# Optimization experiments

Measured on AMD Instinct MI355X. Metric: run time of the kernel, lower is better.

Reference implementation:

```python
import jax, jax.numpy as jnp
import numpy as np

# Dims: B=4, C_in=256, H=W=64 -> L=4096, token_dim D=256, state_dim N=512, K=4
B_, C_IN, H_, W_ = 4, 256, 64, 64
D, N, K = 256, 512, 4


def setup_inputs() -> dict:
    key = jax.random.key(0)
    ks = jax.random.split(key, 16)
    g = lambda k, shape, sc=0.02: (jax.random.normal(k, shape, jnp.float32) * sc)
    return {
        'feat_map': jax.random.normal(ks[0], (B_, C_IN, H_, W_), jnp.float32),
        'hf_map':   jax.random.normal(ks[1], (B_, C_IN, H_, W_), jnp.float32),
        # 1x1 conv proj_f / proj_hf: weight (out=D, in=C_IN), bias (D,)
        'Wf':  g(ks[2], (D, C_IN)), 'bf':  jnp.zeros((D,), jnp.float32),
        'Whf': g(ks[3], (D, C_IN)), 'bhf': jnp.zeros((D,), jnp.float32),
        # alpha_head: Linear(D, D//2) -> GELU -> Linear(D//2, K)
        'Wa1': g(ks[4], (D // 2, D)), 'ba1': jnp.zeros((D // 2,), jnp.float32),
        'Wa2': g(ks[5], (K, D // 2)), 'ba2': jnp.zeros((K,), jnp.float32),
        # SelectiveSSM base tuples: diagonal decay logits A (K,N), input maps B (K,N,D), output maps C (K,D,N)
        'A_base': g(ks[6], (K, N), 1.0),
        'B_base': g(ks[7], (K, N, D), 0.02),
        'C_base': g(ks[8], (K, D, N), 0.02),
        # out_proj 1x1 conv: (C_IN, D)
        'Wout': g(ks[9], (C_IN, D)), 'bout': jnp.zeros((C_IN,), jnp.float32),
    }


def _stage(feat_map, hf_map, Wf, bf, Whf, bhf, Wa1, ba1, Wa2, ba2,
           A_base, B_base, C_base, Wout, bout):
    B, C, H, W = feat_map.shape
    L = H * W
    # 1x1 conv token projections -> (B, L, D)
    t_f = jnp.einsum('bchw,dc->bdhw', feat_map, Wf) + bf[None, :, None, None]
    t_hf = jnp.einsum('bchw,dc->bdhw', hf_map, Whf) + bhf[None, :, None, None]
    x = t_f.reshape(B, -1, L).transpose(0, 2, 1)        # (B, L, D)
    t_hf_seq = t_hf.reshape(B, -1, L).transpose(0, 2, 1)  # (B, L, D)
    # gating MLP -> per-token mixture weights over K base SSMs
    hmid = jax.nn.gelu(t_hf_seq @ Wa1.T + ba1, approximate=False)
    alpha = jax.nn.softmax(hmid @ Wa2.T + ba2, axis=-1)  # (B, L, K)
    # selective SSM: per-token mixed diagonal decay and input drive
    a = jax.nn.sigmoid(jnp.einsum('blk,kn->bln', alpha, A_base))   # (B, L, N)
    u = jnp.einsum('bld,blk,knd->bln', x, alpha, B_base)           # (B, L, N)

    def step(h, au):
        a_t, u_t = au                   # each (B, N)
        h = a_t * h + u_t
        return h, h

    h0 = jnp.zeros((B, a.shape[-1]), x.dtype)
    _, hs = jax.lax.scan(step, h0, (a.transpose(1, 0, 2), u.transpose(1, 0, 2)))
    h_seq = hs.transpose(1, 0, 2)                                   # (B, L, N)
    # mixed readout
    y = jnp.einsum('blk,bln,kdn->bld', alpha, h_seq, C_base)        # (B, L, D)
    y_map = y.transpose(0, 2, 1).reshape(B, -1, H, W)
    out = jnp.einsum('bdhw,cd->bchw', y_map, Wout) + bout[None, :, None, None]
    return out


def reference(feat_map, hf_map, Wf, bf, Whf, bhf, Wa1, ba1, Wa2, ba2,
              A_base, B_base, C_base, Wout, bout):
    return _stage(feat_map, hf_map, Wf, bf, Whf, bhf, Wa1, ba1, Wa2, ba2,
                  A_base, B_base, C_base, Wout, bout)
```

## Files before the change

### kernel.cpp

```cpp
#include <hip/hip_runtime.h>
#include <hip/hip_bf16.h>
#include <math.h>

#define B_  4
#define CIN 256
#define L_  4096
#define D_  256
#define N_  512
#define K_  4
#define DH  128
#define BL  (B_ * L_)

#define NCHUNK 128
#define CLEN   (L_ / NCHUNK)

typedef __attribute__((ext_vector_type(8))) short bfrag;
typedef __attribute__((ext_vector_type(4))) float f4;

__device__ __forceinline__ float bf2f(unsigned short u) {
  return __uint_as_float(((unsigned int)u) << 16);
}
__device__ __forceinline__ unsigned short f2bf(float f) {
  unsigned int u = __float_as_uint(f);
  return (unsigned short)((u + 0x7FFFu + ((u >> 16) & 1u)) >> 16);
}

__global__ void k_prep(const float* __restrict__ Wf, const float* __restrict__ Whf,
                       const float* __restrict__ Wa1, const float* __restrict__ Wout,
                       const float* __restrict__ Bb, const float* __restrict__ Cb,
                       const float* __restrict__ bfv, const float* __restrict__ bhfv,
                       unsigned short* __restrict__ Wfb ,
                       unsigned short* __restrict__ Wa1b,
                       unsigned short* __restrict__ Woutb,
                       unsigned short* __restrict__ Bb16,
                       unsigned short* __restrict__ Cb16,
                       float* __restrict__ biascat) {
  int i = blockIdx.x * 256 + threadIdx.x;
  if (i < 65536) { Wfb[i] = f2bf(Wf[i]); return; } i -= 65536;
  if (i < 65536) { Wfb[65536 + i] = f2bf(Whf[i]); return; } i -= 65536;
  if (i < 32768) { Wa1b[i] = f2bf(Wa1[i]); return; } i -= 32768;
  if (i < 65536) { Woutb[i] = f2bf(Wout[i]); return; } i -= 65536;
  if (i < 524288) {
    int d = i & 255, n = (i >> 8) & 511, k = i >> 17;
    Bb16[(((size_t)n << 2) | k) << 8 | d] = f2bf(Bb[i]);
    return;
  } i -= 524288;
  if (i < 524288) {
    int nn = i & 511, d = (i >> 9) & 255, k = i >> 17;
    Cb16[(((size_t)d << 2) | k) << 9 | nn] = f2bf(Cb[i]);
    return;
  } i -= 524288;
  if (i < 256) { biascat[i] = bfv[i]; return; } i -= 256;
  if (i < 256) { biascat[256 + i] = bhfv[i]; }
}

__global__ void k_transpose2(const float* __restrict__ feat, const float* __restrict__ hf,
                             unsigned short* __restrict__ featT ) {
  __shared__ float tile[32][33];
  const int z = blockIdx.z;
  const int b = z & 3, which = z >> 2;
  const float* in = which ? hf : feat;
  unsigned short* outT = featT + (size_t)which * BL * CIN;
  const int l0 = blockIdx.x * 32, c0 = blockIdx.y * 32;
  const int tx = threadIdx.x, ty = threadIdx.y;
  const float* p = in + ((size_t)b * CIN + c0 + ty) * L_ + l0 + tx;
#pragma unroll
  for (int i = 0; i < 32; i += 8) tile[ty + i][tx] = p[(size_t)i * L_];
  __syncthreads();
  unsigned short* q = outT + ((size_t)b * L_ + l0 + ty) * CIN + c0 + tx;
#pragma unroll
  for (int i = 0; i < 32; i += 8) q[(size_t)i * CIN] = f2bf(tile[tx][ty + i]);
}

__global__ void k_alpha(const float* __restrict__ hm0, const float* __restrict__ hm1,
                        const float* __restrict__ ba1, const float* __restrict__ Wa2,
                        const float* __restrict__ ba2, float* __restrict__ alpha) {
  __shared__ float w2[K_ * DH];
  __shared__ float b1[DH];
  __shared__ float b2[K_];
  for (int i = threadIdx.x; i < K_ * DH; i += 256) w2[i] = Wa2[i];
  if (threadIdx.x < DH) b1[threadIdx.x] = ba1[threadIdx.x];
  if (threadIdx.x < K_) b2[threadIdx.x] = ba2[threadIdx.x];
  __syncthreads();
  const int token = blockIdx.x * 64 + (threadIdx.x >> 2);
  const int q = threadIdx.x & 3;
  float a0 = 0.f, a1 = 0.f, a2 = 0.f, a3 = 0.f;
  const size_t base = (size_t)token * DH + q * 32;
#pragma unroll
  for (int j4 = 0; j4 < 8; ++j4) {
    float4 h0 = *(const float4*)(hm0 + base + j4 * 4);
    float4 h1 = *(const float4*)(hm1 + base + j4 * 4);
    const float hv[4] = {h0.x + h1.x, h0.y + h1.y, h0.z + h1.z, h0.w + h1.w};
#pragma unroll
    for (int e = 0; e < 4; ++e) {
      const int d = q * 32 + j4 * 4 + e;
      float g = hv[e] + b1[d];
      g = 0.5f * g * (1.0f + erff(g * 0.70710678118654752f));
      a0 += g * w2[0 * DH + d];
      a1 += g * w2[1 * DH + d];
      a2 += g * w2[2 * DH + d];
      a3 += g * w2[3 * DH + d];
    }
  }
  a0 += __shfl_xor(a0, 1); a1 += __shfl_xor(a1, 1); a2 += __shfl_xor(a2, 1); a3 += __shfl_xor(a3, 1);
  a0 += __shfl_xor(a0, 2); a1 += __shfl_xor(a1, 2); a2 += __shfl_xor(a2, 2); a3 += __shfl_xor(a3, 2);
  a0 += b2[0]; a1 += b2[1]; a2 += b2[2]; a3 += b2[3];
  float m = fmaxf(fmaxf(a0, a1), fmaxf(a2, a3));
  float e0 = expf(a0 - m), e1 = expf(a1 - m), e2 = expf(a2 - m), e3 = expf(a3 - m);
  float inv = 1.f / (e0 + e1 + e2 + e3);
  float my = (q == 0) ? e0 : (q == 1) ? e1 : (q == 2) ? e2 : e3;
  alpha[(size_t)token * 4 + q] = my * inv;
}


__global__ void k_scanA(const float* __restrict__ u, const float* __restrict__ alpha,
                        const float* __restrict__ Abase,
                        float* __restrict__ P, float* __restrict__ Hend) {
  const int n = threadIdx.x;
  const int bc = blockIdx.x;
  const int b = bc >> 7, c = bc & 127;
  const float A0 = Abase[n], A1 = Abase[N_ + n], A2 = Abase[2 * N_ + n], A3 = Abase[3 * N_ + n];
  const size_t tok0 = (size_t)b * L_ + (size_t)c * CLEN;
  float p = 1.f, h = 0.f;
  for (int l = 0; l < CLEN; ++l) {
    const size_t t = tok0 + l;
    float4 al = *(const float4*)(alpha + t * 4);
    float s = al.x * A0 + al.y * A1 + al.z * A2 + al.w * A3;
    float av = 1.f / (1.f + expf(-s));
    float uv = u[t * N_ + n];
    h = av * h + uv;
    p *= av;
  }
  P[(size_t)bc * N_ + n] = p;
  Hend[(size_t)bc * N_ + n] = h;
}

__global__ void k_scanB(const float* __restrict__ P, const float* __restrict__ Hend,
                        float* __restrict__ Hstart) {
  const int n = threadIdx.x;
  const int b = blockIdx.x;
  float h = 0.f;
  for (int c = 0; c < NCHUNK; ++c) {
    size_t idx = ((size_t)b * NCHUNK + c) * N_ + n;
    Hstart[idx] = h;
    h = P[idx] * h + Hend[idx];
  }
}

__global__ void k_scanC(const float* __restrict__ u, const float* __restrict__ alpha,
                        const float* __restrict__ Abase, const float* __restrict__ Hstart,
                        unsigned short* __restrict__ hbf) {
  const int n = threadIdx.x;
  const int bc = blockIdx.x;
  const int b = bc >> 7, c = bc & 127;
  const float A0 = Abase[n], A1 = Abase[N_ + n], A2 = Abase[2 * N_ + n], A3 = Abase[3 * N_ + n];
  const size_t tok0 = (size_t)b * L_ + (size_t)c * CLEN;
  float h = Hstart[(size_t)bc * N_ + n];
  for (int l = 0; l < CLEN; ++l) {
    const size_t t = tok0 + l;
    float4 al = *(const float4*)(alpha + t * 4);
    float s = al.x * A0 + al.y * A1 + al.z * A2 + al.w * A3;
    float av = 1.f / (1.f + expf(-s));
    float uv = u[t * N_ + n];
    h = av * h + uv;
    hbf[t * N_ + n] = f2bf(h);
  }
}

#define BM 128
#define BN 128
#define BK 32

#define GLL(src, dst)                                                                      \
  __builtin_amdgcn_global_load_lds((const __attribute__((address_space(1))) void*)(src),   \
                                   (__attribute__((address_space(3))) void*)(dst), 16, 0, 0)

template <int BIAS , int EPI >
__global__ __launch_bounds__(256) void gemm_bt(
    const unsigned short* __restrict__ A, long sA,
    const unsigned short* __restrict__ Bm, long sB,
    const float* __restrict__ bias, long bS,
    void* __restrict__ Cv, long sC,
    int M, int N, int Kd, int lda, int ldb) {
  const int zb = blockIdx.z;
  A += (size_t)zb * sA;
  Bm += (size_t)zb * sB;
  if (BIAS) bias += (size_t)zb * bS;
  const int m0 = blockIdx.x * BM;
  const int n0 = blockIdx.y * BN;
  __shared__ __attribute__((aligned(16))) unsigned short As[2 * BM * BK];
  __shared__ __attribute__((aligned(16))) unsigned short Bs[2 * BN * BK];
  const int t = threadIdx.x;
  const int lane = t & 63;
  const int w = t >> 6;
  const int wm = (w >> 1) * 64;
  const int wn = (w & 1) * 64;

  f4 acc[4][4];
#pragma unroll
  for (int i = 0; i < 4; ++i)
#pragma unroll
    for (int j = 0; j < 4; ++j) acc[i][j] = (f4){0.f, 0.f, 0.f, 0.f};

  const int rS = t >> 2;
  const int cS = (t & 3) * 8;
  const unsigned short* gA = A + (size_t)(m0 + rS) * lda + cS;
  const unsigned short* gB = Bm + (size_t)(n0 + rS) * ldb + cS;
  const long rowStepA = (long)64 * lda;
  const long rowStepB = (long)64 * ldb;
  const int kg = (lane >> 4) * 8;
  const int r16 = lane & 15;

#define STAGE1(buf, kt)                                                 \
  do {                                                                  \
    const unsigned short* sA_ = gA + (size_t)(kt) * BK;                 \
    const unsigned short* sB_ = gB + (size_t)(kt) * BK;                 \
    unsigned short* dA_ = As + (buf) * (BM * BK) + t * 8;               \
    unsigned short* dB_ = Bs + (buf) * (BN * BK) + t * 8;               \
    GLL(sA_, dA_); GLL(sA_ + rowStepA, dA_ + 64 * BK);                  \
    GLL(sB_, dB_); GLL(sB_ + rowStepB, dB_ + 64 * BK);                  \
  } while (0)

  const int nIter = Kd / BK;
  STAGE1(0, 0);
  __syncthreads();
  int cur = 0;
  for (int kt = 0; kt < nIter; ++kt) {
    if (kt + 1 < nIter) STAGE1(cur ^ 1, kt + 1);
    const unsigned short* Ab = As + cur * (BM * BK);
    const unsigned short* Bb2 = Bs + cur * (BN * BK);
    bfrag af[4], bfr[4];
#pragma unroll
    for (int i = 0; i < 4; ++i) {
      af[i]  = *(const bfrag*)(Ab + (wm + i * 16 + r16) * BK + kg);
      bfr[i] = *(const bfrag*)(Bb2 + (wn + i * 16 + r16) * BK + kg);
    }
#pragma unroll
    for (int i = 0; i < 4; ++i)
#pragma unroll
      for (int j = 0; j < 4; ++j)
        acc[i][j] = __builtin_amdgcn_mfma_f32_16x16x32_bf16(af[i], bfr[j], acc[i][j], 0, 0, 0);
    __syncthreads();
    cur ^= 1;
  }
#undef STAGE1

  const int rowBase = m0 + wm + ((lane >> 4) << 2);
  const int colBase = n0 + wn + (lane & 15);
  float* Cf = (float*)Cv + (size_t)zb * sC;
  unsigned short* Cb = (unsigned short*)Cv + (size_t)zb * sC;
#pragma unroll
  for (int i = 0; i < 4; ++i) {
#pragma unroll
    for (int j = 0; j < 4; ++j) {
      const int col = colBase + j * 16;
#pragma unroll
      for (int r = 0; r < 4; ++r) {
        const int row = rowBase + i * 16 + r;
        float v = acc[i][j][r];
        if (BIAS == 1) v += bias[col];
        if (BIAS == 2) v += bias[row];
        if (EPI == 1) Cb[(size_t)row * N + col] = f2bf(v);
        else          Cf[(size_t)row * N + col] = v;
      }
    }
  }
}

#define BM2 128
#define BN2 256

template <int BIAS, int EPI>
__global__ __launch_bounds__(512, 2) void gemm_bt2(
    const unsigned short* __restrict__ A, long sA,
    const unsigned short* __restrict__ Bm, long sB,
    const float* __restrict__ bias, long bS,
    const float* __restrict__ alphaP,
    void* __restrict__ Cv, long sC,
    int M, int N, int Kd, int lda, int ldb) {
  const int zb = blockIdx.z;
  A += (size_t)zb * sA;
  Bm += (size_t)zb * sB;
  if (BIAS) bias += (size_t)zb * bS;
  const int m0 = blockIdx.x * BM2;
  const int n0 = blockIdx.y * BN2;
  __shared__ __attribute__((aligned(16))) unsigned short As[3 * BM2 * BK];
  __shared__ __attribute__((aligned(16))) unsigned short Bs[3 * BN2 * BK];
  const int t = threadIdx.x;
  const int lane = t & 63;
  const int w = t >> 6;
  const int wm = (w >> 2) * 64;
  const int wn = (w & 3) * 64;

  f4 acc[4][4];
#pragma unroll
  for (int i = 0; i < 4; ++i)
#pragma unroll
    for (int j = 0; j < 4; ++j) acc[i][j] = (f4){0.f, 0.f, 0.f, 0.f};

  const int rS = t >> 2;
  const int cS = (t & 3) * 8;
  const unsigned short* gA = A + (size_t)(m0 + rS) * lda + cS;
  const unsigned short* gB = Bm + (size_t)(n0 + rS) * ldb + cS;
  const long rowStepB = (long)128 * ldb;
  const int kg = (lane >> 4) * 8;
  const int r16 = lane & 15;

#define STAGE2(slot, kt)                                                \
  do {                                                                  \
    const unsigned short* sA_ = gA + (size_t)(kt) * BK;                 \
    const unsigned short* sB_ = gB + (size_t)(kt) * BK;                 \
    unsigned short* dA_ = As + (slot) * (BM2 * BK) + t * 8;             \
    unsigned short* dB_ = Bs + (slot) * (BN2 * BK) + t * 8;             \
    GLL(sA_, dA_);                                                      \
    GLL(sB_, dB_);                                                      \
    GLL(sB_ + rowStepB, dB_ + BM2 * BK);                                \
  } while (0)

  const int nIter = Kd / BK;
  STAGE2(0, 0);
  STAGE2(1, 1);
  int slot = 0;
  for (int kt = 0; kt < nIter; ++kt) {
    if (kt + 1 < nIter) asm volatile("s_waitcnt vmcnt(3)" ::: "memory");
    else                asm volatile("s_waitcnt vmcnt(0)" ::: "memory");
    __builtin_amdgcn_s_barrier();
    asm volatile("" ::: "memory");
    if (kt + 2 < nIter) {
      int s2 = slot + 2; if (s2 >= 3) s2 -= 3;
      STAGE2(s2, kt + 2);
    }
    const unsigned short* Ab = As + slot * (BM2 * BK);
    const unsigned short* Bb2 = Bs + slot * (BN2 * BK);
    bfrag af[4], bfr[4];
#pragma unroll
    for (int i = 0; i < 4; ++i) {
      af[i]  = *(const bfrag*)(Ab + (wm + i * 16 + r16) * BK + kg);
      bfr[i] = *(const bfrag*)(Bb2 + (wn + i * 16 + r16) * BK + kg);
    }
    __builtin_amdgcn_s_setprio(1);
#pragma unroll
    for (int i = 0; i < 4; ++i)
#pragma unroll
      for (int j = 0; j < 4; ++j)
        acc[i][j] = __builtin_amdgcn_mfma_f32_16x16x32_bf16(af[i], bfr[j], acc[i][j], 0, 0, 0);
    __builtin_amdgcn_s_setprio(0);
    asm volatile("" ::: "memory");
    slot = (slot == 2) ? 0 : slot + 1;
  }
#undef STAGE2

  const int rowBase = m0 + wm + ((lane >> 4) << 2);
  const int colBase = n0 + wn + (lane & 15);

  if (EPI >= 2) {
    const int kq = lane & 3;
    const int NO = N >> 2;
    float av[4][4];
#pragma unroll
    for (int i = 0; i < 4; ++i)
#pragma unroll
      for (int r = 0; r < 4; ++r)
        av[i][r] = alphaP[(size_t)(rowBase + i * 16 + r) * 4 + kq];
    float* Cf = (float*)Cv + (size_t)zb * sC;
    unsigned short* Cb = (unsigned short*)Cv + (size_t)zb * sC;
#pragma unroll
    for (int i = 0; i < 4; ++i)
#pragma unroll
      for (int j = 0; j < 4; ++j) {
        const int col = colBase + j * 16;
#pragma unroll
        for (int r = 0; r < 4; ++r) {
          float p = av[i][r] * acc[i][j][r];
          p += __shfl_xor(p, 1);
          p += __shfl_xor(p, 2);
          if (kq == 0) {
            const int row = rowBase + i * 16 + r;
            if (EPI == 2) Cf[(size_t)row * NO + (col >> 2)] = p;
            else          Cb[(size_t)row * NO + (col >> 2)] = f2bf(p);
          }
        }
      }
    return;
  }

  float* Cf = (float*)Cv + (size_t)zb * sC;
  unsigned short* Cb = (unsigned short*)Cv + (size_t)zb * sC;
#pragma unroll
  for (int i = 0; i < 4; ++i) {
#pragma unroll
    for (int j = 0; j < 4; ++j) {
      const int col = colBase + j * 16;
#pragma unroll
      for (int r = 0; r < 4; ++r) {
        const int row = rowBase + i * 16 + r;
        float v = acc[i][j][r];
        if (BIAS == 1) v += bias[col];
        if (BIAS == 2) v += bias[row];
        if (EPI == 1) Cb[(size_t)row * N + col] = f2bf(v);
        else          Cf[(size_t)row * N + col] = v;
      }
    }
  }
}


extern "C" void kernel_launch(void* const* d_in, const int* in_sizes, int n_in,
                              void* d_out, int out_size, void* d_ws, size_t ws_size,
                              hipStream_t stream) {
  const float* feat  = (const float*)d_in[0];
  const float* hf    = (const float*)d_in[1];
  const float* Wf    = (const float*)d_in[2];
  const float* bfv   = (const float*)d_in[3];
  const float* Whf   = (const float*)d_in[4];
  const float* bhfv  = (const float*)d_in[5];
  const float* Wa1   = (const float*)d_in[6];
  const float* ba1   = (const float*)d_in[7];
  const float* Wa2   = (const float*)d_in[8];
  const float* ba2   = (const float*)d_in[9];
  const float* Abase = (const float*)d_in[10];
  const float* Bbase = (const float*)d_in[11];
  const float* Cbase = (const float*)d_in[12];
  const float* Wout  = (const float*)d_in[13];
  const float* bout  = (const float*)d_in[14];
  float* out = (float*)d_out;

  char* ws = (char*)d_ws;
  size_t off = 0;
  auto alloc = [&](size_t bytes) { void* p = ws + off; off += bytes; return p; };

  unsigned short* Wfb    = (unsigned short*)alloc((size_t)2 * D_ * CIN * 2);
  unsigned short* Wa1b   = (unsigned short*)alloc((size_t)DH * D_ * 2);
  unsigned short* Woutb  = (unsigned short*)alloc((size_t)CIN * D_ * 2);
  unsigned short* Bb16   = (unsigned short*)alloc((size_t)K_ * N_ * D_ * 2);
  unsigned short* Cb16   = (unsigned short*)alloc((size_t)K_ * D_ * N_ * 2);
  float*          biascat= (float*)alloc((size_t)2 * D_ * 4);
  float*          alpha  = (float*)alloc((size_t)BL * K_ * 4);
  float*          Pc     = (float*)alloc((size_t)B_ * NCHUNK * N_ * 4);
  float*          He     = (float*)alloc((size_t)B_ * NCHUNK * N_ * 4);
  float*          Hs     = (float*)alloc((size_t)B_ * NCHUNK * N_ * 4);
  unsigned short* hbf    = (unsigned short*)alloc((size_t)BL * N_ * 2);
  unsigned short* x      = (unsigned short*)alloc((size_t)BL * D_ * 2);
  unsigned short* thf    = (unsigned short*)alloc((size_t)BL * D_ * 2);
  unsigned short* featT  = (unsigned short*)alloc((size_t)BL * CIN * 2);
  unsigned short* hfT    = (unsigned short*)alloc((size_t)BL * CIN * 2);
  float*          u      = (float*)alloc((size_t)BL * N_ * 4);

  float*          hm0 = (float*)featT;
  float*          hm1 = (float*)hfT;
  unsigned short* y   = thf;

  if (ws_size < off) return;

  k_prep<<<dim3((3 * 65536 + 32768 + 2 * 524288 + 512 + 255) / 256), 256, 0, stream>>>(
      Wf, Whf, Wa1, Wout, Bbase, Cbase, bfv, bhfv, Wfb, Wa1b, Woutb, Bb16, Cb16, biascat);

  k_transpose2<<<dim3(L_ / 32, CIN / 32, 2 * B_), dim3(32, 8), 0, stream>>>(feat, hf, featT);

  gemm_bt2<1, 1><<<dim3(BL / BM2, D_ / BN2, 2), 512, 0, stream>>>(
      featT, (long)BL * CIN, Wfb, (long)D_ * CIN, biascat, D_, nullptr,
      x, (long)BL * D_, BL, D_, CIN, CIN, CIN);

  gemm_bt<0, 0><<<dim3(BL / BM, DH / BN, 2), 256, 0, stream>>>(
      thf, 128, Wa1b, 128, nullptr, 0,
      hm0, (long)BL * DH, BL, DH, 128, D_, D_);
  k_alpha<<<dim3(BL / 64), 256, 0, stream>>>(hm0, hm1, ba1, Wa2, ba2, alpha);

  gemm_bt2<0, 2><<<dim3(BL / BM2, (K_ * N_) / BN2, 1), 512, 0, stream>>>(
      x, 0, Bb16, 0, nullptr, 0, alpha, u, 0, BL, K_ * N_, D_, D_, D_);

  k_scanA<<<dim3(B_ * NCHUNK), N_, 0, stream>>>(u, alpha, Abase, Pc, He);
  k_scanB<<<dim3(B_), N_, 0, stream>>>(Pc, He, Hs);
  k_scanC<<<dim3(B_ * NCHUNK), N_, 0, stream>>>(u, alpha, Abase, Hs, hbf);

  gemm_bt2<0, 3><<<dim3(BL / BM2, (K_ * D_) / BN2, 1), 512, 0, stream>>>(
      hbf, 0, Cb16, 0, nullptr, 0, alpha, y, 0, BL, K_ * D_, N_, N_, N_);

  gemm_bt<2, 0><<<dim3(CIN / BM, L_ / BN, B_), 256, 0, stream>>>(
      Woutb, 0, y, (long)L_ * D_, bout, 0, out, (long)CIN * L_, CIN, L_, D_, D_, D_);
}
```

Measured before the change: 163.9 us.

## Store SSM drive u in bf16 and triple-buffer the small GEMMs

```diff
diff --git a/kernel.cpp b/kernel.cpp
--- a/kernel.cpp
+++ b/kernel.cpp
@@ -113,7 +113,7 @@
 }
 
 
-__global__ void k_scanA(const float* __restrict__ u, const float* __restrict__ alpha,
+__global__ void k_scanA(const unsigned short* __restrict__ u, const float* __restrict__ alpha,
                         const float* __restrict__ Abase,
                         float* __restrict__ P, float* __restrict__ Hend) {
   const int n = threadIdx.x;
@@ -127,7 +127,7 @@
     float4 al = *(const float4*)(alpha + t * 4);
     float s = al.x * A0 + al.y * A1 + al.z * A2 + al.w * A3;
     float av = 1.f / (1.f + expf(-s));
-    float uv = u[t * N_ + n];
+    float uv = bf2f(u[t * N_ + n]);
     h = av * h + uv;
     p *= av;
   }
@@ -147,7 +147,7 @@
   }
 }
 
-__global__ void k_scanC(const float* __restrict__ u, const float* __restrict__ alpha,
+__global__ void k_scanC(const unsigned short* __restrict__ u, const float* __restrict__ alpha,
                         const float* __restrict__ Abase, const float* __restrict__ Hstart,
                         unsigned short* __restrict__ hbf) {
   const int n = threadIdx.x;
@@ -161,7 +161,7 @@
     float4 al = *(const float4*)(alpha + t * 4);
     float s = al.x * A0 + al.y * A1 + al.z * A2 + al.w * A3;
     float av = 1.f / (1.f + expf(-s));
-    float uv = u[t * N_ + n];
+    float uv = bf2f(u[t * N_ + n]);
     h = av * h + uv;
     hbf[t * N_ + n] = f2bf(h);
   }
@@ -174,98 +174,6 @@
 #define GLL(src, dst)                                                                      \
   __builtin_amdgcn_global_load_lds((const __attribute__((address_space(1))) void*)(src),   \
                                    (__attribute__((address_space(3))) void*)(dst), 16, 0, 0)
-
-template <int BIAS , int EPI >
-__global__ __launch_bounds__(256) void gemm_bt(
-    const unsigned short* __restrict__ A, long sA,
-    const unsigned short* __restrict__ Bm, long sB,
-    const float* __restrict__ bias, long bS,
-    void* __restrict__ Cv, long sC,
-    int M, int N, int Kd, int lda, int ldb) {
-  const int zb = blockIdx.z;
-  A += (size_t)zb * sA;
-  Bm += (size_t)zb * sB;
-  if (BIAS) bias += (size_t)zb * bS;
-  const int m0 = blockIdx.x * BM;
-  const int n0 = blockIdx.y * BN;
-  __shared__ __attribute__((aligned(16))) unsigned short As[2 * BM * BK];
-  __shared__ __attribute__((aligned(16))) unsigned short Bs[2 * BN * BK];
-  const int t = threadIdx.x;
-  const int lane = t & 63;
-  const int w = t >> 6;
-  const int wm = (w >> 1) * 64;
-  const int wn = (w & 1) * 64;
-
-  f4 acc[4][4];
-#pragma unroll
-  for (int i = 0; i < 4; ++i)
-#pragma unroll
-    for (int j = 0; j < 4; ++j) acc[i][j] = (f4){0.f, 0.f, 0.f, 0.f};
-
-  const int rS = t >> 2;
-  const int cS = (t & 3) * 8;
-  const unsigned short* gA = A + (size_t)(m0 + rS) * lda + cS;
-  const unsigned short* gB = Bm + (size_t)(n0 + rS) * ldb + cS;
-  const long rowStepA = (long)64 * lda;
-  const long rowStepB = (long)64 * ldb;
-  const int kg = (lane >> 4) * 8;
-  const int r16 = lane & 15;
-
-#define STAGE1(buf, kt)                                                 \
-  do {                                                                  \
-    const unsigned short* sA_ = gA + (size_t)(kt) * BK;                 \
-    const unsigned short* sB_ = gB + (size_t)(kt) * BK;                 \
-    unsigned short* dA_ = As + (buf) * (BM * BK) + t * 8;               \
-    unsigned short* dB_ = Bs + (buf) * (BN * BK) + t * 8;               \
-    GLL(sA_, dA_); GLL(sA_ + rowStepA, dA_ + 64 * BK);                  \
-    GLL(sB_, dB_); GLL(sB_ + rowStepB, dB_ + 64 * BK);                  \
-  } while (0)
-
-  const int nIter = Kd / BK;
-  STAGE1(0, 0);
-  __syncthreads();
-  int cur = 0;
-  for (int kt = 0; kt < nIter; ++kt) {
-    if (kt + 1 < nIter) STAGE1(cur ^ 1, kt + 1);
-    const unsigned short* Ab = As + cur * (BM * BK);
-    const unsigned short* Bb2 = Bs + cur * (BN * BK);
-    bfrag af[4], bfr[4];
-#pragma unroll
-    for (int i = 0; i < 4; ++i) {
-      af[i]  = *(const bfrag*)(Ab + (wm + i * 16 + r16) * BK + kg);
-      bfr[i] = *(const bfrag*)(Bb2 + (wn + i * 16 + r16) * BK + kg);
-    }
-#pragma unroll
-    for (int i = 0; i < 4; ++i)
-#pragma unroll
-      for (int j = 0; j < 4; ++j)
-        acc[i][j] = __builtin_amdgcn_mfma_f32_16x16x32_bf16(af[i], bfr[j], acc[i][j], 0, 0, 0);
-    __syncthreads();
-    cur ^= 1;
-  }
-#undef STAGE1
-
-  const int rowBase = m0 + wm + ((lane >> 4) << 2);
-  const int colBase = n0 + wn + (lane & 15);
-  float* Cf = (float*)Cv + (size_t)zb * sC;
-  unsigned short* Cb = (unsigned short*)Cv + (size_t)zb * sC;
-#pragma unroll
-  for (int i = 0; i < 4; ++i) {
-#pragma unroll
-    for (int j = 0; j < 4; ++j) {
-      const int col = colBase + j * 16;
-#pragma unroll
-      for (int r = 0; r < 4; ++r) {
-        const int row = rowBase + i * 16 + r;
-        float v = acc[i][j][r];
-        if (BIAS == 1) v += bias[col];
-        if (BIAS == 2) v += bias[row];
-        if (EPI == 1) Cb[(size_t)row * N + col] = f2bf(v);
-        else          Cf[(size_t)row * N + col] = v;
-      }
-    }
-  }
-}
 
 #define BM2 128
 #define BN2 256
@@ -404,6 +312,107 @@
   }
 }
 
+template <int BIAS, int EPI >
+__global__ __launch_bounds__(256) void gemm_bt3(
+    const unsigned short* __restrict__ A, long sA,
+    const unsigned short* __restrict__ Bm, long sB,
+    const float* __restrict__ bias, long bS,
+    void* __restrict__ Cv, long sC,
+    int M, int N, int Kd, int lda, int ldb) {
+  const int zb = blockIdx.z;
+  A += (size_t)zb * sA;
+  Bm += (size_t)zb * sB;
+  if (BIAS) bias += (size_t)zb * bS;
+  const int m0 = blockIdx.x * BM;
+  const int n0 = blockIdx.y * BN;
+  __shared__ __attribute__((aligned(16))) unsigned short As[3 * BM * BK];
+  __shared__ __attribute__((aligned(16))) unsigned short Bs[3 * BN * BK];
+  const int t = threadIdx.x;
+  const int lane = t & 63;
+  const int w = t >> 6;
+  const int wm = (w >> 1) * 64;
+  const int wn = (w & 1) * 64;
+
+  f4 acc[4][4];
+#pragma unroll
+  for (int i = 0; i < 4; ++i)
+#pragma unroll
+    for (int j = 0; j < 4; ++j) acc[i][j] = (f4){0.f, 0.f, 0.f, 0.f};
+
+  const int rS = t >> 2;
+  const int cS = (t & 3) * 8;
+  const unsigned short* gA = A + (size_t)(m0 + rS) * lda + cS;
+  const unsigned short* gB = Bm + (size_t)(n0 + rS) * ldb + cS;
+  const long rowStepA = (long)64 * lda;
+  const long rowStepB = (long)64 * ldb;
+  const int kg = (lane >> 4) * 8;
+  const int r16 = lane & 15;
+
+#define STAGE3(slot, kt)                                                \
+  do {                                                                  \
+    const unsigned short* sA_ = gA + (size_t)(kt) * BK;                 \
+    const unsigned short* sB_ = gB + (size_t)(kt) * BK;                 \
+    unsigned short* dA_ = As + (slot) * (BM * BK) + t * 8;              \
+    unsigned short* dB_ = Bs + (slot) * (BN * BK) + t * 8;              \
+    GLL(sA_, dA_); GLL(sA_ + rowStepA, dA_ + 64 * BK);                  \
+    GLL(sB_, dB_); GLL(sB_ + rowStepB, dB_ + 64 * BK);                  \
+  } while (0)
+
+  const int nIter = Kd / BK;
+  STAGE3(0, 0);
+  STAGE3(1, 1);
+  int slot = 0;
+  for (int kt = 0; kt < nIter; ++kt) {
+    if (kt + 1 < nIter) asm volatile("s_waitcnt vmcnt(4)" ::: "memory");
+    else                asm volatile("s_waitcnt vmcnt(0)" ::: "memory");
+    __builtin_amdgcn_s_barrier();
+    asm volatile("" ::: "memory");
+    if (kt + 2 < nIter) {
+      int s2 = slot + 2; if (s2 >= 3) s2 -= 3;
+      STAGE3(s2, kt + 2);
+    }
+    const unsigned short* Ab = As + slot * (BM * BK);
+    const unsigned short* Bb2 = Bs + slot * (BN * BK);
+    bfrag af[4], bfr[4];
+#pragma unroll
+    for (int i = 0; i < 4; ++i) {
+      af[i]  = *(const bfrag*)(Ab + (wm + i * 16 + r16) * BK + kg);
+      bfr[i] = *(const bfrag*)(Bb2 + (wn + i * 16 + r16) * BK + kg);
+    }
+    __builtin_amdgcn_s_setprio(1);
+#pragma unroll
+    for (int i = 0; i < 4; ++i)
+#pragma unroll
+      for (int j = 0; j < 4; ++j)
+        acc[i][j] = __builtin_amdgcn_mfma_f32_16x16x32_bf16(af[i], bfr[j], acc[i][j], 0, 0, 0);
+    __builtin_amdgcn_s_setprio(0);
+    asm volatile("" ::: "memory");
+    slot = (slot == 2) ? 0 : slot + 1;
+  }
+#undef STAGE3
+
+  const int rowBase = m0 + wm + ((lane >> 4) << 2);
+  const int colBase = n0 + wn + (lane & 15);
+  float* Cf = (float*)Cv + (size_t)zb * sC;
+  unsigned short* Cb = (unsigned short*)Cv + (size_t)zb * sC;
+#pragma unroll
+  for (int i = 0; i < 4; ++i) {
+#pragma unroll
+    for (int j = 0; j < 4; ++j) {
+      const int col = colBase + j * 16;
+#pragma unroll
+      for (int r = 0; r < 4; ++r) {
+        const int row = rowBase + i * 16 + r;
+        float v = acc[i][j][r];
+        if (BIAS == 1) v += bias[col];
+        if (BIAS == 2) v += bias[row];
+        if (EPI == 1) Cb[(size_t)row * N + col] = f2bf(v);
+        else          Cf[(size_t)row * N + col] = v;
+      }
+    }
+  }
+}
+
 
 extern "C" void kernel_launch(void* const* d_in, const int* in_sizes, int n_in,
                               void* d_out, int out_size, void* d_ws, size_t ws_size,
@@ -444,7 +453,7 @@
   unsigned short* thf    = (unsigned short*)alloc((size_t)BL * D_ * 2);
   unsigned short* featT  = (unsigned short*)alloc((size_t)BL * CIN * 2);
   unsigned short* hfT    = (unsigned short*)alloc((size_t)BL * CIN * 2);
-  float*          u      = (float*)alloc((size_t)BL * N_ * 4);
+  unsigned short* u16    = (unsigned short*)alloc((size_t)BL * N_ * 2);
 
   float*          hm0 = (float*)featT;
   float*          hm1 = (float*)hfT;
@@ -461,21 +470,21 @@
       featT, (long)BL * CIN, Wfb, (long)D_ * CIN, biascat, D_, nullptr,
       x, (long)BL * D_, BL, D_, CIN, CIN, CIN);
 
-  gemm_bt<0, 0><<<dim3(BL / BM, DH / BN, 2), 256, 0, stream>>>(
+  gemm_bt3<0, 0><<<dim3(BL / BM, DH / BN, 2), 256, 0, stream>>>(
       thf, 128, Wa1b, 128, nullptr, 0,
       hm0, (long)BL * DH, BL, DH, 128, D_, D_);
   k_alpha<<<dim3(BL / 64), 256, 0, stream>>>(hm0, hm1, ba1, Wa2, ba2, alpha);
 
-  gemm_bt2<0, 2><<<dim3(BL / BM2, (K_ * N_) / BN2, 1), 512, 0, stream>>>(
-      x, 0, Bb16, 0, nullptr, 0, alpha, u, 0, BL, K_ * N_, D_, D_, D_);
-
-  k_scanA<<<dim3(B_ * NCHUNK), N_, 0, stream>>>(u, alpha, Abase, Pc, He);
+  gemm_bt2<0, 3><<<dim3(BL / BM2, (K_ * N_) / BN2, 1), 512, 0, stream>>>(
+      x, 0, Bb16, 0, nullptr, 0, alpha, u16, 0, BL, K_ * N_, D_, D_, D_);
+
+  k_scanA<<<dim3(B_ * NCHUNK), N_, 0, stream>>>(u16, alpha, Abase, Pc, He);
   k_scanB<<<dim3(B_), N_, 0, stream>>>(Pc, He, Hs);
-  k_scanC<<<dim3(B_ * NCHUNK), N_, 0, stream>>>(u, alpha, Abase, Hs, hbf);
+  k_scanC<<<dim3(B_ * NCHUNK), N_, 0, stream>>>(u16, alpha, Abase, Hs, hbf);
 
   gemm_bt2<0, 3><<<dim3(BL / BM2, (K_ * D_) / BN2, 1), 512, 0, stream>>>(
       hbf, 0, Cb16, 0, nullptr, 0, alpha, y, 0, BL, K_ * D_, N_, N_, N_);
 
-  gemm_bt<2, 0><<<dim3(CIN / BM, L_ / BN, B_), 256, 0, stream>>>(
+  gemm_bt3<2, 0><<<dim3(CIN / BM, L_ / BN, B_), 256, 0, stream>>>(
       Woutb, 0, y, (long)L_ * D_, bout, 0, out, (long)CIN * L_, CIN, L_, D_, D_, D_);
 }
```

After: 162.0 us. About the same (-1.2%).
